# Optimization experiments

Measured on AMD Instinct MI355X. Metric: run time of the kernel, lower is better.

## Reference

```python
import jax, jax.numpy as jnp
import numpy as np


def setup_inputs() -> dict:
    key = jax.random.key(0)
    k1, k2, k3 = jax.random.split(key, 3)
    B, S, H, E = 4, 4096, 7168, 256
    return {
        "hidden_states": jax.random.normal(k1, (B, S, H), dtype=jnp.float32),
        "gate_weight": jax.random.normal(k2, (E, H), dtype=jnp.float32) * (H ** -0.5),
        "bias": jax.random.normal(k3, (E,), dtype=jnp.float32) * 0.01,
        "n_group": 8,
        "topk_group": 4,
        "top_k": 8,
    }


def reference(hidden_states, gate_weight, bias, n_group, topk_group, top_k):
    B, S, H = hidden_states.shape
    E = gate_weight.shape[0]
    group_size = E // n_group
    x = hidden_states.reshape(-1, H)  # [T, H]
    logits = jnp.einsum("th,eh->te", x, gate_weight)  # [T, E]
    scores = jax.nn.sigmoid(logits) + bias  # [T, E]
    scores_g = scores.reshape(-1, n_group, group_size)  # [T, G, E/G]
    group_scores = scores_g.max(axis=-1)  # [T, G]
    _, sel_groups = jax.lax.top_k(group_scores, topk_group)  # [T, topk_group]
    # group mask: 1.0 for selected groups (indices are distinct, so sum of one-hots is 0/1)
    group_mask = jax.nn.one_hot(sel_groups, n_group, dtype=scores.dtype).sum(axis=1)  # [T, G]
    masked = (scores_g * group_mask[:, :, None]).reshape(-1, E)  # [T, E]
    weights, indices = jax.lax.top_k(masked, top_k)  # [T, top_k]
    weights = weights / (weights.sum(axis=-1, keepdims=True) + 1e-6)
    return weights.reshape(B, S, -1), indices.reshape(B, S, -1)
```

## Files before the change

kernel.cpp:

```cpp
#include <hip/hip_runtime.h>


#define TTOK 16384
#define EEXP 256
#define HDIM 7168
#define BM 128
#define BE 128
#define BK 32
#define SPLITK 2
#define KSLICE (HDIM / SPLITK)
#define NSTEP (KSLICE / BK)
#define NTHR 512
#define LDS_BYTES 65536
#define EPI_LDS (64 * 257 * 4)

typedef __attribute__((ext_vector_type(4))) float f32x4;
typedef __attribute__((ext_vector_type(8))) _Float16 h8;

__device__ __forceinline__ void gload_lds16(const void* g, void* l) {
  typedef const __attribute__((address_space(1))) unsigned int gu32;
  typedef __attribute__((address_space(3))) unsigned int lu32;
  __builtin_amdgcn_global_load_lds((gu32*)g, (lu32*)l, 16, 0, 0);
}

__global__ __launch_bounds__(64) void pack_w_kernel(const float* __restrict__ W,
                                                    _Float16* __restrict__ blob) {
  const int kcg = blockIdx.x;
  const int eb = blockIdx.y;
  const int lane = threadIdx.x;
  const int e = eb * 16 + (lane & 15);
  const int k0 = kcg * 32 + (lane >> 4) * 8;
  const float* src = W + (size_t)e * HDIM + k0;
  h8 hi, lo;
#pragma unroll
  for (int j = 0; j < 8; ++j) {
    float x = src[j];
    _Float16 h = (_Float16)x;
    hi[j] = h;
    lo[j] = (_Float16)((x - (float)h) * 2048.0f);
  }
  const int slice = kcg / NSTEP, kcl = kcg % NSTEP;
  const int ehalf = eb >> 3, ebl = eb & 7;
  char* dst = (char*)blob + ((size_t)(slice * 2 + ehalf) * NSTEP + kcl) * 16384 +
              (ebl * 2) * 1024 + lane * 16;
  *(h8*)dst = hi;
  *(h8*)(dst + 1024) = lo;
}

__global__ __launch_bounds__(NTHR, 4) void gate_kernel(
    const float* __restrict__ X, const _Float16* __restrict__ Wblob,
    float* __restrict__ part) {
  extern __shared__ char smem[];

  const int bid = blockIdx.x;
  const int slice = (bid & 7) >> 2;
  const int ehalf = (bid >> 3) & 1;
  const int tb = ((bid >> 4) << 2) | (bid & 3);
  const int tok0 = tb * BM;
  const int kbase = slice * KSLICE;
  const char* blobs = (const char*)Wblob +
                      ((size_t)(slice * 2 + ehalf) * NSTEP) * 16384;

  const int tid = threadIdx.x;
  const int lane = tid & 63;
  const int wid = tid >> 6;
  const int wr = wid >> 1;
  const int wc = wid & 1;

  f32x4 ra[2];

  f32x4 acc1[2][4], acc2[2][4];
#pragma unroll
  for (int m = 0; m < 2; ++m)
#pragma unroll
    for (int n = 0; n < 4; ++n) {
      acc1[m][n] = (f32x4){0.f, 0.f, 0.f, 0.f};
      acc2[m][n] = (f32x4){0.f, 0.f, 0.f, 0.f};
    }

  auto LOADA = [&](int T) {
    const float* p = X + (size_t)(tok0 + (tid >> 2)) * HDIM + kbase + T * BK +
                     (tid & 3) * 8;
    ra[0] = *(const f32x4*)p;
    ra[1] = *(const f32x4*)(p + 4);
  };

  auto STAGEB = [&](int T, int buf) {
    const char* gs = blobs + (size_t)T * 16384 + lane * 16;
    char* lb = smem + buf * 16384 + lane * 16;
    gload_lds16(gs + (wid * 2) * 1024, lb + (wid * 2) * 1024);
    gload_lds16(gs + (wid * 2 + 1) * 1024, lb + (wid * 2 + 1) * 1024);
  };

  auto STOREA = [&](int buf) {
    h8 hi, lo;
#pragma unroll
    for (int half = 0; half < 2; ++half) {
      const f32x4 v = ra[half];
#pragma unroll
      for (int j = 0; j < 4; ++j) {
        const float x = v[j];
        const _Float16 h = (_Float16)x;
        hi[half * 4 + j] = h;
        lo[half * 4 + j] = (_Float16)((x - (float)h) * 2048.0f);
      }
    }
    char* ah = smem + 32768 + buf * 16384;
    const int row = tid >> 2, q = tid & 3;
    *(h8*)(ah + q * 2048 + row * 16) = hi;
    *(h8*)(ah + 8192 + q * 2048 + row * 16) = lo;
  };

  auto PHASE = [&](int buf) {
    const char* ahp = smem + 32768 + buf * 16384;
    const char* bb = smem + buf * 16384;
    h8 ah[2], al[2];
#pragma unroll
    for (int m = 0; m < 2; ++m) {
      const int r_ = wr * 32 + m * 16 + (lane & 15);
      const int ao_ = (lane >> 4) * 2048 + r_ * 16;
      ah[m] = *(const h8*)(ahp + ao_);
      al[m] = *(const h8*)(ahp + 8192 + ao_);
    }
    __builtin_amdgcn_s_setprio(1);
#pragma unroll
    for (int n = 0; n < 4; ++n) {
      const int bo_ = ((wc * 4 + n) * 2) * 1024 + lane * 16;
      const h8 bh = *(const h8*)(bb + bo_);
      const h8 bl = *(const h8*)(bb + bo_ + 1024);
#pragma unroll
      for (int m = 0; m < 2; ++m) {
        acc1[m][n] = __builtin_amdgcn_mfma_f32_16x16x32_f16(ah[m], bh, acc1[m][n], 0, 0, 0);
        acc2[m][n] = __builtin_amdgcn_mfma_f32_16x16x32_f16(ah[m], bl, acc2[m][n], 0, 0, 0);
        acc2[m][n] = __builtin_amdgcn_mfma_f32_16x16x32_f16(al[m], bh, acc2[m][n], 0, 0, 0);
      }
    }
    __builtin_amdgcn_s_setprio(0);
  };

  LOADA(0);
  asm volatile("" ::: "memory");
  STAGEB(0, 0);
  asm volatile("" ::: "memory");
  STOREA(0);
  LOADA(1);
  asm volatile("s_waitcnt vmcnt(2) lgkmcnt(0)" ::: "memory");
  __builtin_amdgcn_s_barrier();

  int p = 0;
#pragma unroll 1
  for (int T = 0; T < NSTEP; ++T) {
    if (T + 1 < NSTEP) {
      STAGEB(T + 1, p ^ 1);
      asm volatile("" ::: "memory");
      STOREA(p ^ 1);
      if (T + 2 < NSTEP) LOADA(T + 2);
    }
    PHASE(p);
    if (T + 2 < NSTEP) {
      asm volatile("s_waitcnt vmcnt(2) lgkmcnt(0)" ::: "memory");
    } else {
      asm volatile("s_waitcnt vmcnt(0) lgkmcnt(0)" ::: "memory");
    }
    __builtin_amdgcn_s_barrier();
    p ^= 1;
  }

  float* pbase = part + ((size_t)slice * TTOK + tok0) * EEXP + ehalf * BE;
#pragma unroll
  for (int m = 0; m < 2; ++m)
#pragma unroll
    for (int n = 0; n < 4; ++n) {
      const int e = wc * 64 + n * 16 + (lane & 15);
      const int t0 = wr * 32 + m * 16 + (lane >> 4) * 4;
#pragma unroll
      for (int r = 0; r < 4; ++r)
        pbase[(size_t)(t0 + r) * EEXP + e] =
            acc1[m][n][r] + acc2[m][n][r] * (1.0f / 2048.0f);
    }
}

__global__ __launch_bounds__(256) void epilogue_kernel(
    const float* __restrict__ part, const float* __restrict__ bias,
    float* __restrict__ outw, float* __restrict__ outi) {
  extern __shared__ float sc[];
  const int tid = threadIdx.x;
  const long t0 = (long)blockIdx.x * 64;

  const int e4 = (tid & 63) * 4;
  const int rsub = tid >> 6;
  const f32x4 bv = *(const f32x4*)(bias + e4);
#pragma unroll
  for (int rr = 0; rr < 16; ++rr) {
    const int row = rr * 4 + rsub;
    const f32x4 a = *(const f32x4*)(part + (t0 + row) * EEXP + e4);
    const f32x4 c = *(const f32x4*)(part + ((long)TTOK + t0 + row) * EEXP + e4);
#pragma unroll
    for (int j = 0; j < 4; ++j) {
      const float v = a[j] + c[j];
      sc[row * 257 + e4 + j] = 1.0f / (1.0f + expf(-v)) + bv[j];
    }
  }
  __syncthreads();

  if (tid < 64) {
    const float* s = sc + tid * 257;
    float gmax[8];
#pragma unroll
    for (int g = 0; g < 8; ++g) {
      float mx = -1e30f;
      for (int j = 0; j < 32; ++j) mx = fmaxf(mx, s[g * 32 + j]);
      gmax[g] = mx;
    }
    unsigned selmask = 0;
    for (int it = 0; it < 4; ++it) {
      float best = -1e30f;
      int bi = 0;
      for (int g = 0; g < 8; ++g)
        if (!((selmask >> g) & 1) && gmax[g] > best) {
          best = gmax[g];
          bi = g;
        }
      selmask |= 1u << bi;
    }
    float vals[8];
    int idx[8];
#pragma unroll
    for (int j = 0; j < 8; ++j) {
      vals[j] = -1e30f;
      idx[j] = 0;
    }
    for (int e = 0; e < 256; ++e) {
      const float v = ((selmask >> (e >> 5)) & 1) ? s[e] : 0.0f;
      if (v > vals[7]) {
        int p = 7;
        while (p > 0 && v > vals[p - 1]) {
          vals[p] = vals[p - 1];
          idx[p] = idx[p - 1];
          --p;
        }
        vals[p] = v;
        idx[p] = e;
      }
    }
    float ssum = 0.0f;
#pragma unroll
    for (int j = 0; j < 8; ++j) ssum += vals[j];
    const float den = ssum + 1e-6f;
    const long tg = t0 + tid;
#pragma unroll
    for (int j = 0; j < 8; ++j) {
      outw[tg * 8 + j] = vals[j] / den;
      outi[tg * 8 + j] = (float)idx[j];
    }
  }
}

extern "C" void kernel_launch(void* const* d_in, const int* in_sizes, int n_in,
                              void* d_out, int out_size, void* d_ws, size_t ws_size,
                              hipStream_t stream) {
  const float* X = (const float*)d_in[0];
  const float* W = (const float*)d_in[1];
  const float* bias = (const float*)d_in[2];

  _Float16* wblob = (_Float16*)d_ws;
  float* part = (float*)((char*)d_ws + (size_t)EEXP * HDIM * 4);

  float* outw = (float*)d_out;
  float* outi = outw + (size_t)TTOK * 8;

  hipFuncSetAttribute((const void*)gate_kernel,
                      hipFuncAttributeMaxDynamicSharedMemorySize, LDS_BYTES);
  hipFuncSetAttribute((const void*)epilogue_kernel,
                      hipFuncAttributeMaxDynamicSharedMemorySize, EPI_LDS);

  pack_w_kernel<<<dim3(HDIM / 32, EEXP / 16), 64, 0, stream>>>(W, wblob);
  gate_kernel<<<SPLITK * 2 * (TTOK / BM), NTHR, LDS_BYTES, stream>>>(X, wblob, part);
  epilogue_kernel<<<TTOK / 64, 256, EPI_LDS, stream>>>(part, bias, outw, outi);
}
```

Baseline: 299.3 us.

## Triple-buffer B tiles in LDS to prefetch weights two steps ahead

Expands LDS to hold three B (weight) buffers plus two A buffers, so global-to-LDS loads of weights are issued two K-steps ahead. The A conversion and store now happen after the MFMA phase, with a looser vmcnt wait so more loads stay in flight. This is meant to hide global load latency better. The cost is LDS growing from 64KB to 80KB per block, which can cut how many blocks fit on a CU and lower the intended occupancy of four.

```diff
diff --git a/kernel.cpp b/kernel.cpp
--- a/kernel.cpp
+++ b/kernel.cpp
@@ -11,7 +11,8 @@
 #define KSLICE (HDIM / SPLITK)
 #define NSTEP (KSLICE / BK)
 #define NTHR 512
-#define LDS_BYTES 65536
+#define LDS_BYTES 81920
+#define ABASE 49152
 #define EPI_LDS (64 * 257 * 4)
 
 typedef __attribute__((ext_vector_type(4))) float f32x4;
@@ -105,15 +106,15 @@
         lo[half * 4 + j] = (_Float16)((x - (float)h) * 2048.0f);
       }
     }
-    char* ah = smem + 32768 + buf * 16384;
+    char* ah = smem + ABASE + buf * 16384;
     const int row = tid >> 2, q = tid & 3;
     *(h8*)(ah + q * 2048 + row * 16) = hi;
     *(h8*)(ah + 8192 + q * 2048 + row * 16) = lo;
   };
 
-  auto PHASE = [&](int buf) {
-    const char* ahp = smem + 32768 + buf * 16384;
-    const char* bb = smem + buf * 16384;
+  auto PHASE = [&](int pa, int pb) {
+    const char* ahp = smem + ABASE + pa * 16384;
+    const char* bb = smem + pb * 16384;
     h8 ah[2], al[2];
 #pragma unroll
     for (int m = 0; m < 2; ++m) {
@@ -138,32 +139,35 @@
     __builtin_amdgcn_s_setprio(0);
   };
 
+  STAGEB(0, 0);
   LOADA(0);
-  asm volatile("" ::: "memory");
-  STAGEB(0, 0);
-  asm volatile("" ::: "memory");
+  STAGEB(1, 1);
   STOREA(0);
   LOADA(1);
-  asm volatile("s_waitcnt vmcnt(2) lgkmcnt(0)" ::: "memory");
+  asm volatile("s_waitcnt vmcnt(4) lgkmcnt(0)" ::: "memory");
   __builtin_amdgcn_s_barrier();
 
-  int p = 0;
+  int pa = 0, pb = 0;
 #pragma unroll 1
   for (int T = 0; T < NSTEP; ++T) {
+    const bool p2 = (T + 2 < NSTEP);
+    if (p2) {
+      int sb = pb + 2;
+      if (sb >= 3) sb -= 3;
+      STAGEB(T + 2, sb);
+    }
+    PHASE(pa, pb);
     if (T + 1 < NSTEP) {
-      STAGEB(T + 1, p ^ 1);
-      asm volatile("" ::: "memory");
-      STOREA(p ^ 1);
-      if (T + 2 < NSTEP) LOADA(T + 2);
-    }
-    PHASE(p);
-    if (T + 2 < NSTEP) {
-      asm volatile("s_waitcnt vmcnt(2) lgkmcnt(0)" ::: "memory");
-    } else {
-      asm volatile("s_waitcnt vmcnt(0) lgkmcnt(0)" ::: "memory");
-    }
-    __builtin_amdgcn_s_barrier();
-    p ^= 1;
+      STOREA(pa ^ 1);
+      if (p2) LOADA(T + 2);
+      if (p2)
+        asm volatile("s_waitcnt vmcnt(4) lgkmcnt(0)" ::: "memory");
+      else
+        asm volatile("s_waitcnt vmcnt(0) lgkmcnt(0)" ::: "memory");
+      __builtin_amdgcn_s_barrier();
+    }
+    pa ^= 1;
+    pb = (pb == 2) ? 0 : pb + 1;
   }
 
   float* pbase = part + ((size_t)slice * TTOK + tok0) * EEXP + ehalf * BE;
```

After: 292.2 us. 2.4% less time.
